# Kernel tuning notes

Hardware: AMD Instinct MI355X
Metric: run time of the kernel (lower is better)

## Reference

```python
import jax, jax.numpy as jnp
import numpy as np

DIM = 512
HEADS = 8
DIM_HEAD = 64
INNER = HEADS * DIM_HEAD  # 512
EPS = 1e-5
SCALE = DIM_HEAD ** (-0.5)


def setup_inputs() -> dict:
    key = jax.random.key(0)
    ks = jax.random.split(key, 12)
    B, S = 8, 1024
    x = jax.random.normal(ks[0], (B, DIM, S, 1), dtype=jnp.float32)
    # BatchNorm2d params (eval mode: running stats)
    bn_gamma = jax.random.normal(ks[1], (DIM,), dtype=jnp.float32) * 0.1 + 1.0
    bn_beta = jax.random.normal(ks[2], (DIM,), dtype=jnp.float32) * 0.1
    bn_mean = jax.random.normal(ks[3], (DIM,), dtype=jnp.float32) * 0.1
    bn_var = jax.random.uniform(ks[4], (DIM,), dtype=jnp.float32, minval=0.5, maxval=1.5)
    # 1x1 Conv2d == linear: weight [out, in], bias [out]
    def lin(k, out_d, in_d):
        kw, kb = jax.random.split(k)
        lim = 1.0 / np.sqrt(in_d)
        w = jax.random.uniform(kw, (out_d, in_d), dtype=jnp.float32, minval=-lim, maxval=lim)
        b = jax.random.uniform(kb, (out_d,), dtype=jnp.float32, minval=-lim, maxval=lim)
        return w, b
    wq, bq = lin(ks[5], INNER, DIM)
    wk, bk = lin(ks[6], INNER, DIM)
    wv, bv = lin(ks[7], INNER, DIM)
    wo, bo = lin(ks[8], DIM, INNER)
    return {"x": x, "bn_gamma": bn_gamma, "bn_beta": bn_beta,
            "bn_mean": bn_mean, "bn_var": bn_var,
            "wq": wq, "bq": bq, "wk": wk, "bk": bk,
            "wv": wv, "bv": bv, "wo": wo, "bo": bo}


def reference(x, bn_gamma, bn_beta, bn_mean, bn_var,
              wq, bq, wk, bk, wv, bv, wo, bo):
    B, C, S, _ = x.shape
    # BatchNorm2d (eval) over channel dim
    inv = jax.lax.rsqrt(bn_var + EPS)
    xn = (x - bn_mean[None, :, None, None]) * (bn_gamma * inv)[None, :, None, None] \
         + bn_beta[None, :, None, None]
    t = jnp.transpose(xn[..., 0], (0, 2, 1))  # [B, S, C]
    q = (t @ wq.T + bq).reshape(B, S, HEADS, DIM_HEAD)
    k = (t @ wk.T + bk).reshape(B, S, HEADS, DIM_HEAD)
    v = (t @ wv.T + bv).reshape(B, S, HEADS, DIM_HEAD)
    scores = jnp.einsum('bshd,bthd->bhst', q, k) * SCALE  # [B,H,S,S]
    attn = jax.nn.softmax(scores, axis=-1)
    o = jnp.einsum('bhst,bthd->bshd', attn, v).reshape(B, S, INNER)
    y = o @ wo.T + bo  # [B, S, C]
    return jnp.transpose(y, (0, 2, 1))[..., None]  # [B, C, S, 1]
```

## Files before the change

### kernel.cpp

```cpp
#include <hip/hip_runtime.h>
#include <stdint.h>

typedef __bf16 bf16;
typedef bf16 bf16x8 __attribute__((ext_vector_type(8)));
typedef bf16 bf16x4 __attribute__((ext_vector_type(4)));
typedef float f32x4 __attribute__((ext_vector_type(4)));
typedef float f32x16 __attribute__((ext_vector_type(16)));

#define NB 8
#define NS 1024
#define NC 512
#define NH 8
#define ND 64

#define QSCALE 0.18033688011f

__device__ __forceinline__ void gload16(const void* g, void* l) {
  __builtin_amdgcn_global_load_lds(
      (const __attribute__((address_space(1))) void*)g,
      (__attribute__((address_space(3))) void*)l, 16, 0, 0);
}

__device__ __forceinline__ unsigned pk2(float lo, float hi) {
  union { bf16 h[2]; unsigned u; } c;
  c.h[0] = (bf16)lo;
  c.h[1] = (bf16)hi;
  return c.u;
}

__device__ __forceinline__ void plswap(unsigned& x, unsigned& y) {
#if __has_builtin(__builtin_amdgcn_permlane32_swap)
  typedef unsigned uint2v __attribute__((ext_vector_type(2)));
  uint2v r = __builtin_amdgcn_permlane32_swap(x, y, false, false);
  x = r[0];
  y = r[1];
#else
  const bool hi = (threadIdx.x & 32) != 0;
  const unsigned xs = (unsigned)__shfl_xor((int)x, 32);
  const unsigned ys = (unsigned)__shfl_xor((int)y, 32);
  const unsigned nx = hi ? ys : x;
  const unsigned ny = hi ? y : xs;
  x = nx;
  y = ny;
#endif
}

__global__ __launch_bounds__(256) void prep_kernel(
    const float* __restrict__ x, const float* __restrict__ gam,
    const float* __restrict__ bet, const float* __restrict__ mu,
    const float* __restrict__ var, const float* __restrict__ wq,
    const float* __restrict__ wk, const float* __restrict__ wv,
    const float* __restrict__ wo, bf16* __restrict__ t, bf16* __restrict__ wqb,
    bf16* __restrict__ wkb, bf16* __restrict__ wvb, bf16* __restrict__ wob) {
  __shared__ float tile[32][33];
  const int bid = blockIdx.x;
  if (bid < 4096) {
    const int b = bid >> 9, c0 = ((bid >> 5) & 15) << 5, s0 = (bid & 31) << 5;
    const int tx = threadIdx.x, sj = tx & 31, ci = tx >> 5;
#pragma unroll
    for (int kk = 0; kk < 4; ++kk) {
      const int c = c0 + ci + (kk << 3);
      const float sc = gam[c] * rsqrtf(var[c] + 1e-5f);
      const float sh = bet[c] - mu[c] * sc;
      tile[ci + (kk << 3)][sj] = x[(size_t)(b * NC + c) * NS + s0 + sj] * sc + sh;
    }
    __syncthreads();
#pragma unroll
    for (int kk = 0; kk < 4; ++kk) {
      const int s = s0 + ci + (kk << 3);
      t[(size_t)(b * NS + s) * NC + c0 + sj] = (bf16)tile[sj][ci + (kk << 3)];
    }
  } else {
    const int i = ((bid - 4096) * 256 + threadIdx.x) * 4;
    float4 a = *(const float4*)(&wq[i]);
    float4 b = *(const float4*)(&wk[i]);
    float4 c = *(const float4*)(&wv[i]);
    float4 d = *(const float4*)(&wo[i]);
    bf16x4 av = {(bf16)a.x, (bf16)a.y, (bf16)a.z, (bf16)a.w};
    bf16x4 bv = {(bf16)b.x, (bf16)b.y, (bf16)b.z, (bf16)b.w};
    bf16x4 cv = {(bf16)c.x, (bf16)c.y, (bf16)c.z, (bf16)c.w};
    bf16x4 dv = {(bf16)d.x, (bf16)d.y, (bf16)d.z, (bf16)d.w};
    *(bf16x4*)(&wqb[i]) = av;
    *(bf16x4*)(&wkb[i]) = bv;
    *(bf16x4*)(&wvb[i]) = cv;
    *(bf16x4*)(&wob[i]) = dv;
  }
}

__global__ __launch_bounds__(256) void gemm_qkv_kernel(
    const bf16* __restrict__ t, const bf16* __restrict__ wqb,
    const bf16* __restrict__ wkb, const bf16* __restrict__ wvb,
    const float* __restrict__ bq, const float* __restrict__ bk,
    const float* __restrict__ bv, bf16* __restrict__ qo, bf16* __restrict__ ko,
    bf16* __restrict__ vo) {
  __shared__ __align__(16) bf16 As[2][128 * 32];
  __shared__ __align__(16) bf16 Bs[2][128 * 32];
  const int lid = blockIdx.x;
  const int xcd = lid & 7, rr = lid >> 3;
  const int ny = rr % 12, mx = (rr / 12) * 8 + xcd;
  const int m0 = mx << 7, n0 = ny << 7;
  const int tid = threadIdx.x;
  const int wsel = n0 >> 9;
  const bf16* W = (wsel == 0) ? wqb : (wsel == 1 ? wkb : wvb);
  const float* bias = (wsel == 0) ? bq : (wsel == 1 ? bk : bv);
  const int nb = n0 & 511;
  const int w = tid >> 6, lane = tid & 63, l15 = lane & 15, l4 = lane >> 4;
  const int wm = (w >> 1) << 6, wn = (w & 1) << 6;

  const int srl = lane >> 2, sp = lane & 3;
  const int r0 = w * 16 + srl, r1 = 64 + w * 16 + srl;
  const int c0off = (sp ^ ((r0 >> 1) & 3)) << 3;
  const int c1off = (sp ^ ((r1 >> 1) & 3)) << 3;
  const bf16* a0 = t + (size_t)(m0 + r0) * 512 + c0off;
  const bf16* a1 = t + (size_t)(m0 + r1) * 512 + c1off;
  const bf16* b0 = W + (size_t)(nb + r0) * 512 + c0off;
  const bf16* b1 = W + (size_t)(nb + r1) * 512 + c1off;

  f32x4 acc[4][4] = {};
  gload16(a0, &As[0][w * 512]);
  gload16(a1, &As[0][2048 + w * 512]);
  gload16(b0, &Bs[0][w * 512]);
  gload16(b1, &Bs[0][2048 + w * 512]);
  __syncthreads();
  int buf = 0;
  for (int k0 = 0; k0 < 512; k0 += 32, buf ^= 1) {
    if (k0 + 32 < 512) {
      gload16(a0 + k0 + 32, &As[buf ^ 1][w * 512]);
      gload16(a1 + k0 + 32, &As[buf ^ 1][2048 + w * 512]);
      gload16(b0 + k0 + 32, &Bs[buf ^ 1][w * 512]);
      gload16(b1 + k0 + 32, &Bs[buf ^ 1][2048 + w * 512]);
    }
    bf16x8 af[4], bfv[4];
#pragma unroll
    for (int mi = 0; mi < 4; ++mi) {
      const int row = wm + mi * 16 + l15;
      af[mi] = *(const bf16x8*)(&As[buf][row * 32 + ((l4 ^ ((row >> 1) & 3)) << 3)]);
    }
#pragma unroll
    for (int ni = 0; ni < 4; ++ni) {
      const int row = wn + ni * 16 + l15;
      bfv[ni] = *(const bf16x8*)(&Bs[buf][row * 32 + ((l4 ^ ((row >> 1) & 3)) << 3)]);
    }
    if (wsel == 2) {
#pragma unroll
      for (int mi = 0; mi < 4; ++mi)
#pragma unroll
        for (int ni = 0; ni < 4; ++ni)
          acc[mi][ni] = __builtin_amdgcn_mfma_f32_16x16x32_bf16(
              af[mi], bfv[ni], acc[mi][ni], 0, 0, 0);
    } else {
#pragma unroll
      for (int mi = 0; mi < 4; ++mi)
#pragma unroll
        for (int ni = 0; ni < 4; ++ni)
          acc[mi][ni] = __builtin_amdgcn_mfma_f32_16x16x32_bf16(
              bfv[ni], af[mi], acc[mi][ni], 0, 0, 0);
    }
    __syncthreads();
  }
  const int bidx = m0 >> 10;
  if (wsel == 2) {
    const int sbase = (m0 & 1023) + wm + (l4 << 2);
#pragma unroll
    for (int ni = 0; ni < 4; ++ni) {
      const int nn = nb + wn + ni * 16 + l15;
      const int hh = nn >> 6, dd = nn & 63;
      const float bsv = bias[nn];
      bf16* vbase = vo + (size_t)(bidx * NH + hh) * (ND * NS) + (size_t)dd * NS + sbase;
#pragma unroll
      for (int mi = 0; mi < 4; ++mi) {
        bf16x4 pk;
#pragma unroll
        for (int r = 0; r < 4; ++r) pk[r] = (bf16)(acc[mi][ni][r] + bsv);
        *(bf16x4*)(&vbase[mi * 16]) = pk;
      }
    }
  } else {
    const bool isq = (wsel == 0);
    bf16* outp = isq ? qo : ko;
    const int sbase = (m0 & 1023) + wm + l15;
#pragma unroll
    for (int ni = 0; ni < 4; ++ni) {
      const int nn0 = nb + wn + ni * 16 + (l4 << 2);
      const int hh = nn0 >> 6, dd0 = nn0 & 63;
      const float4 bs4 = *(const float4*)(&bias[nn0]);
      bf16* obase = outp + (size_t)(bidx * NH + hh) * (NS * ND) + dd0;
#pragma unroll
      for (int mi = 0; mi < 4; ++mi) {
        bf16x4 pk;
        const float* bp = (const float*)&bs4;
#pragma unroll
        for (int r = 0; r < 4; ++r) {
          float val = acc[mi][ni][r] + bp[r];
          if (isq) val *= QSCALE;
          pk[r] = (bf16)val;
        }
        *(bf16x4*)(&obase[(size_t)(sbase + mi * 16) * ND]) = pk;
      }
    }
  }
}

__global__ __launch_bounds__(256, 2) void attn_kernel(
    const bf16* __restrict__ qg, const bf16* __restrict__ kg,
    const bf16* __restrict__ vtg, bf16* __restrict__ og) {
  __shared__ __align__(16) bf16 Kb[2][64 * 64];
  __shared__ __align__(16) bf16 Vb[2][64 * 64];
  const int lid = blockIdx.x;
  const int xcd = lid & 7, rr = lid >> 3;
  const int bh = ((rr & 7) << 3) + xcd;
  const int q0 = (rr >> 3) << 7;
  const int tid = threadIdx.x, w = tid >> 6, lane = tid & 63;
  const int l31 = lane & 31, hi = lane >> 5;
  const bf16* Qp = qg + ((size_t)bh * NS + q0) * ND;
  const bf16* Kp = kg + (size_t)bh * NS * ND;
  const bf16* Vp = vtg + (size_t)bh * ND * NS;

  bf16x8 qf0, qf1, qf2, qf3;
  {
    const bf16* qrow = Qp + (size_t)(w * 32 + l31) * ND + hi * 8;
    qf0 = *(const bf16x8*)(qrow);
    qf1 = *(const bf16x8*)(qrow + 16);
    qf2 = *(const bf16x8*)(qrow + 32);
    qf3 = *(const bf16x8*)(qrow + 48);
  }

  const int srow = w * 16 + (lane >> 3);
  const int sslot = (lane & 7) ^ (srow & 7);
  const bf16* ksrc = Kp + (size_t)srow * ND + sslot * 8;
  const bf16* vsrc = Vp + (size_t)srow * NS + sslot * 8;

  f32x16 oacc0 = {}, oacc1 = {};
  float mrun = -1e30f, lrun = 0.f;

  gload16(ksrc, &Kb[0][w * 1024]);
  gload16(ksrc + 8 * ND, &Kb[0][w * 1024 + 512]);
  gload16(vsrc, &Vb[0][w * 1024]);
  gload16(vsrc + 8 * NS, &Vb[0][w * 1024 + 512]);
  __syncthreads();

  const int s7 = l31 & 7;
  int buf = 0;
  for (int kv0 = 0; kv0 < NS; kv0 += 64, buf ^= 1) {
    if (kv0 + 64 < NS) {
      gload16(ksrc + (size_t)(kv0 + 64) * ND, &Kb[buf ^ 1][w * 1024]);
      gload16(ksrc + (size_t)(kv0 + 72) * ND, &Kb[buf ^ 1][w * 1024 + 512]);
      gload16(vsrc + kv0 + 64, &Vb[buf ^ 1][w * 1024]);
      gload16(vsrc + 8 * NS + kv0 + 64, &Vb[buf ^ 1][w * 1024 + 512]);
    }
    const bf16* Ks = Kb[buf];
    const bf16* Vs = Vb[buf];
    f32x16 st0 = {}, st1 = {};
    __builtin_amdgcn_s_setprio(1);
#pragma unroll
    for (int ks = 0; ks < 4; ++ks) {
      const int sl = ((2 * ks + hi) ^ s7) << 3;
      const bf16x8 a0 = *(const bf16x8*)(&Ks[l31 * 64 + sl]);
      const bf16x8 a1 = *(const bf16x8*)(&Ks[(32 + l31) * 64 + sl]);
      const bf16x8 qk = (ks == 0) ? qf0 : (ks == 1) ? qf1 : (ks == 2) ? qf2 : qf3;
      st0 = __builtin_amdgcn_mfma_f32_32x32x16_bf16(a0, qk, st0, 0, 0, 0);
      st1 = __builtin_amdgcn_mfma_f32_32x32x16_bf16(a1, qk, st1, 0, 0, 0);
    }
    __builtin_amdgcn_s_setprio(0);
    float pm = st0[0];
#pragma unroll
    for (int i = 1; i < 16; ++i) pm = fmaxf(pm, st0[i]);
#pragma unroll
    for (int i = 0; i < 16; ++i) pm = fmaxf(pm, st1[i]);
    pm = fmaxf(pm, __shfl_xor(pm, 32));
    if (!__all(pm - mrun <= 8.f)) {
      const float mnew = fmaxf(mrun, pm);
      const float alpha = __builtin_amdgcn_exp2f(mrun - mnew);
#pragma unroll
      for (int i = 0; i < 16; ++i) {
        oacc0[i] *= alpha;
        oacc1[i] *= alpha;
      }
      lrun *= alpha;
      mrun = mnew;
    }
    float rs = 0.f;
#pragma unroll
    for (int t = 0; t < 4; ++t) {
      float p[8];
#pragma unroll
      for (int i = 0; i < 8; ++i) {
        const float sv = (t < 2) ? st0[8 * (t & 1) + i] : st1[8 * (t & 1) + i];
        p[i] = __builtin_amdgcn_exp2f(sv - mrun);
        rs += p[i];
      }
      unsigned c01 = pk2(p[0], p[1]), c23 = pk2(p[2], p[3]);
      unsigned c45 = pk2(p[4], p[5]), c67 = pk2(p[6], p[7]);
      plswap(c01, c45);
      plswap(c23, c67);
      union { unsigned u[4]; bf16x8 v; } pu;
      pu.u[0] = c01;
      pu.u[1] = c23;
      pu.u[2] = c45;
      pu.u[3] = c67;
      const int sl = ((2 * t + hi) ^ s7) << 3;
      const bf16x8 v0 = *(const bf16x8*)(&Vs[l31 * 64 + sl]);
      const bf16x8 v1 = *(const bf16x8*)(&Vs[(32 + l31) * 64 + sl]);
      __builtin_amdgcn_s_setprio(1);
      oacc0 = __builtin_amdgcn_mfma_f32_32x32x16_bf16(v0, pu.v, oacc0, 0, 0, 0);
      oacc1 = __builtin_amdgcn_mfma_f32_32x32x16_bf16(v1, pu.v, oacc1, 0, 0, 0);
      __builtin_amdgcn_s_setprio(0);
    }
    lrun += rs;
    __syncthreads();
  }
  lrun += __shfl_xor(lrun, 32);
  const float linv = 1.f / lrun;
  const int b = bh >> 3, h = bh & 7;
  bf16* Op = og + (size_t)(b * NS + q0 + w * 32 + l31) * NC + h * ND;
#pragma unroll
  for (int g = 0; g < 4; ++g) {
    bf16x4 pk0, pk1;
#pragma unroll
    for (int r = 0; r < 4; ++r) {
      pk0[r] = (bf16)(oacc0[4 * g + r] * linv);
      pk1[r] = (bf16)(oacc1[4 * g + r] * linv);
    }
    *(bf16x4*)(&Op[g * 8 + 4 * hi]) = pk0;
    *(bf16x4*)(&Op[32 + g * 8 + 4 * hi]) = pk1;
  }
}

__global__ __launch_bounds__(256) void gemm_out_kernel(
    const bf16* __restrict__ wob, const bf16* __restrict__ o,
    const float* __restrict__ bo, float* __restrict__ out) {
  __shared__ __align__(16) bf16 As[2][64 * 32];
  __shared__ __align__(16) bf16 Bs[2][128 * 32];
  const int lid = blockIdx.x;
  const int xcd = lid & 7, rr = lid >> 3;
  const int mx = rr & 7, ny = ((rr >> 3) << 3) + xcd;
  const int m0 = mx << 6, n0 = ny << 7;
  const int tid = threadIdx.x;
  const int w = tid >> 6, lane = tid & 63, l15 = lane & 15, l4 = lane >> 4;
  const int wm = (w >> 1) << 5;
  const int wn = (w & 1) << 6;

  const int srl = lane >> 2, sp = lane & 3;
  const int ra = w * 16 + srl;
  const int caoff = (sp ^ ((ra >> 1) & 3)) << 3;
  const bf16* a0 = wob + (size_t)(m0 + ra) * 512 + caoff;
  const int rb0 = w * 16 + srl, rb1 = 64 + w * 16 + srl;
  const int cb0off = (sp ^ ((rb0 >> 1) & 3)) << 3;
  const int cb1off = (sp ^ ((rb1 >> 1) & 3)) << 3;
  const bf16* b0 = o + (size_t)(n0 + rb0) * 512 + cb0off;
  const bf16* b1 = o + (size_t)(n0 + rb1) * 512 + cb1off;

  f32x4 acc[2][4] = {};
  gload16(a0, &As[0][w * 512]);
  gload16(b0, &Bs[0][w * 512]);
  gload16(b1, &Bs[0][2048 + w * 512]);
  __syncthreads();
  int buf = 0;
  for (int k0 = 0; k0 < 512; k0 += 32, buf ^= 1) {
    if (k0 + 32 < 512) {
      gload16(a0 + k0 + 32, &As[buf ^ 1][w * 512]);
      gload16(b0 + k0 + 32, &Bs[buf ^ 1][w * 512]);
      gload16(b1 + k0 + 32, &Bs[buf ^ 1][2048 + w * 512]);
    }
    bf16x8 af[2], bfv[4];
#pragma unroll
    for (int mi = 0; mi < 2; ++mi) {
      const int row = wm + mi * 16 + l15;
      af[mi] = *(const bf16x8*)(&As[buf][row * 32 + ((l4 ^ ((row >> 1) & 3)) << 3)]);
    }
#pragma unroll
    for (int ni = 0; ni < 4; ++ni) {
      const int row = wn + ni * 16 + l15;
      bfv[ni] = *(const bf16x8*)(&Bs[buf][row * 32 + ((l4 ^ ((row >> 1) & 3)) << 3)]);
    }
#pragma unroll
    for (int mi = 0; mi < 2; ++mi)
#pragma unroll
      for (int ni = 0; ni < 4; ++ni)
        acc[mi][ni] = __builtin_amdgcn_mfma_f32_16x16x32_bf16(
            bfv[ni], af[mi], acc[mi][ni], 0, 0, 0);
    __syncthreads();
  }
  const int b = n0 >> 10;
  const int sb = (n0 & 1023) + wn;
#pragma unroll
  for (int mi = 0; mi < 2; ++mi) {
    const int cout = m0 + wm + mi * 16 + l15;
    const float bsv = bo[cout];
    float* obase = out + (size_t)(b * NC + cout) * NS;
#pragma unroll
    for (int ni = 0; ni < 4; ++ni) {
      const int s0i = sb + ni * 16 + (l4 << 2);
      float4 pk = {acc[mi][ni][0] + bsv, acc[mi][ni][1] + bsv,
                   acc[mi][ni][2] + bsv, acc[mi][ni][3] + bsv};
      *(float4*)(&obase[s0i]) = pk;
    }
  }
}

extern "C" void kernel_launch(void* const* d_in, const int* in_sizes, int n_in,
                              void* d_out, int out_size, void* d_ws,
                              size_t ws_size, hipStream_t stream) {
  const float* x = (const float*)d_in[0];
  const float* gam = (const float*)d_in[1];
  const float* bet = (const float*)d_in[2];
  const float* mu = (const float*)d_in[3];
  const float* var = (const float*)d_in[4];
  const float* wq = (const float*)d_in[5];
  const float* bq = (const float*)d_in[6];
  const float* wk = (const float*)d_in[7];
  const float* bk = (const float*)d_in[8];
  const float* wv = (const float*)d_in[9];
  const float* bv = (const float*)d_in[10];
  const float* wo = (const float*)d_in[11];
  const float* bo = (const float*)d_in[12];
  float* out = (float*)d_out;

  char* p = (char*)d_ws;
  const size_t big = (size_t)8192 * 512 * sizeof(bf16);
  bf16* t = (bf16*)p;   p += big;
  bf16* q = (bf16*)p;   p += big;
  bf16* k = (bf16*)p;   p += big;
  bf16* vt = (bf16*)p;  p += big;
  const size_t wsz = (size_t)512 * 512 * sizeof(bf16);
  bf16* wqb = (bf16*)p; p += wsz;
  bf16* wkb = (bf16*)p; p += wsz;
  bf16* wvb = (bf16*)p; p += wsz;
  bf16* wob = (bf16*)p; p += wsz;
  bf16* o = t;

  prep_kernel<<<dim3(4352), 256, 0, stream>>>(x, gam, bet, mu, var, wq, wk, wv,
                                              wo, t, wqb, wkb, wvb, wob);
  gemm_qkv_kernel<<<dim3(768), 256, 0, stream>>>(t, wqb, wkb, wvb, bq, bk, bv,
                                                 q, k, vt);
  attn_kernel<<<dim3(512), 256, 0, stream>>>(q, k, vt, o);
  gemm_out_kernel<<<dim3(512), 256, 0, stream>>>(wob, o, bo, out);
}
```

Baseline: 86.43 us.

## Load K/V fragments directly from global into registers in attention, drop LDS staging

The attention kernel no longer stages K and V tiles in shared memory with double buffering and barriers. Each wave now loads its MFMA operand fragments straight from global memory into registers, prefetching the next K tile during softmax with ping-pong register arrays. The aim is to remove LDS traffic and __syncthreads, but each of the four waves now fetches the same K/V data separately, which raises global/L2 traffic and register pressure. The QKV GEMM also gets a launch-bounds occupancy hint of 3.

```diff
diff --git a/kernel.cpp b/kernel.cpp
--- a/kernel.cpp
+++ b/kernel.cpp
@@ -87,7 +87,7 @@
   }
 }
 
-__global__ __launch_bounds__(256) void gemm_qkv_kernel(
+__global__ __launch_bounds__(256, 3) void gemm_qkv_kernel(
     const bf16* __restrict__ t, const bf16* __restrict__ wqb,
     const bf16* __restrict__ wkb, const bf16* __restrict__ wvb,
     const float* __restrict__ bq, const float* __restrict__ bk,
@@ -204,8 +204,6 @@
 __global__ __launch_bounds__(256, 2) void attn_kernel(
     const bf16* __restrict__ qg, const bf16* __restrict__ kg,
     const bf16* __restrict__ vtg, bf16* __restrict__ og) {
-  __shared__ __align__(16) bf16 Kb[2][64 * 64];
-  __shared__ __align__(16) bf16 Vb[2][64 * 64];
   const int lid = blockIdx.x;
   const int xcd = lid & 7, rr = lid >> 3;
   const int bh = ((rr & 7) << 3) + xcd;
@@ -213,55 +211,50 @@
   const int tid = threadIdx.x, w = tid >> 6, lane = tid & 63;
   const int l31 = lane & 31, hi = lane >> 5;
   const bf16* Qp = qg + ((size_t)bh * NS + q0) * ND;
-  const bf16* Kp = kg + (size_t)bh * NS * ND;
-  const bf16* Vp = vtg + (size_t)bh * ND * NS;
-
-  bf16x8 qf0, qf1, qf2, qf3;
+  const bf16* kb = kg + (size_t)bh * NS * ND + (size_t)l31 * ND + hi * 8;
+  const bf16* vb = vtg + (size_t)bh * ND * NS + (size_t)l31 * NS + hi * 8;
+  const bf16* vb2 = vb + (size_t)32 * NS;
+
+  bf16x8 qf[4];
   {
     const bf16* qrow = Qp + (size_t)(w * 32 + l31) * ND + hi * 8;
-    qf0 = *(const bf16x8*)(qrow);
-    qf1 = *(const bf16x8*)(qrow + 16);
-    qf2 = *(const bf16x8*)(qrow + 32);
-    qf3 = *(const bf16x8*)(qrow + 48);
-  }
-
-  const int srow = w * 16 + (lane >> 3);
-  const int sslot = (lane & 7) ^ (srow & 7);
-  const bf16* ksrc = Kp + (size_t)srow * ND + sslot * 8;
-  const bf16* vsrc = Vp + (size_t)srow * NS + sslot * 8;
+#pragma unroll
+    for (int ks = 0; ks < 4; ++ks) qf[ks] = *(const bf16x8*)(qrow + ks * 16);
+  }
 
   f32x16 oacc0 = {}, oacc1 = {};
   float mrun = -1e30f, lrun = 0.f;
 
-  gload16(ksrc, &Kb[0][w * 1024]);
-  gload16(ksrc + 8 * ND, &Kb[0][w * 1024 + 512]);
-  gload16(vsrc, &Vb[0][w * 1024]);
-  gload16(vsrc + 8 * NS, &Vb[0][w * 1024 + 512]);
-  __syncthreads();
-
-  const int s7 = l31 & 7;
-  int buf = 0;
-  for (int kv0 = 0; kv0 < NS; kv0 += 64, buf ^= 1) {
-    if (kv0 + 64 < NS) {
-      gload16(ksrc + (size_t)(kv0 + 64) * ND, &Kb[buf ^ 1][w * 1024]);
-      gload16(ksrc + (size_t)(kv0 + 72) * ND, &Kb[buf ^ 1][w * 1024 + 512]);
-      gload16(vsrc + kv0 + 64, &Vb[buf ^ 1][w * 1024]);
-      gload16(vsrc + 8 * NS + kv0 + 64, &Vb[buf ^ 1][w * 1024 + 512]);
-    }
-    const bf16* Ks = Kb[buf];
-    const bf16* Vs = Vb[buf];
+  bf16x8 kA0[4], kA1[4], kB0[4], kB1[4];
+#pragma unroll
+  for (int ks = 0; ks < 4; ++ks) {
+    kA0[ks] = *(const bf16x8*)(kb + ks * 16);
+    kA1[ks] = *(const bf16x8*)(kb + (size_t)32 * ND + ks * 16);
+  }
+
+  auto tile = [&](const bf16x8 (&kc0)[4], const bf16x8 (&kc1)[4],
+                  bf16x8 (&kn0)[4], bf16x8 (&kn1)[4], int kv0) {
+    bf16x8 vf0[4], vf1[4];
+#pragma unroll
+    for (int t = 0; t < 4; ++t) {
+      vf0[t] = *(const bf16x8*)(vb + kv0 + t * 16);
+      vf1[t] = *(const bf16x8*)(vb2 + kv0 + t * 16);
+    }
     f32x16 st0 = {}, st1 = {};
     __builtin_amdgcn_s_setprio(1);
 #pragma unroll
     for (int ks = 0; ks < 4; ++ks) {
-      const int sl = ((2 * ks + hi) ^ s7) << 3;
-      const bf16x8 a0 = *(const bf16x8*)(&Ks[l31 * 64 + sl]);
-      const bf16x8 a1 = *(const bf16x8*)(&Ks[(32 + l31) * 64 + sl]);
-      const bf16x8 qk = (ks == 0) ? qf0 : (ks == 1) ? qf1 : (ks == 2) ? qf2 : qf3;
-      st0 = __builtin_amdgcn_mfma_f32_32x32x16_bf16(a0, qk, st0, 0, 0, 0);
-      st1 = __builtin_amdgcn_mfma_f32_32x32x16_bf16(a1, qk, st1, 0, 0, 0);
+      st0 = __builtin_amdgcn_mfma_f32_32x32x16_bf16(kc0[ks], qf[ks], st0, 0, 0, 0);
+      st1 = __builtin_amdgcn_mfma_f32_32x32x16_bf16(kc1[ks], qf[ks], st1, 0, 0, 0);
     }
     __builtin_amdgcn_s_setprio(0);
+    if (kv0 + 64 < NS) {
+#pragma unroll
+      for (int ks = 0; ks < 4; ++ks) {
+        kn0[ks] = *(const bf16x8*)(kb + (size_t)(kv0 + 64) * ND + ks * 16);
+        kn1[ks] = *(const bf16x8*)(kb + (size_t)(kv0 + 96) * ND + ks * 16);
+      }
+    }
     float pm = st0[0];
 #pragma unroll
     for (int i = 1; i < 16; ++i) pm = fmaxf(pm, st0[i]);
@@ -298,17 +291,19 @@
       pu.u[1] = c23;
       pu.u[2] = c45;
       pu.u[3] = c67;
-      const int sl = ((2 * t + hi) ^ s7) << 3;
-      const bf16x8 v0 = *(const bf16x8*)(&Vs[l31 * 64 + sl]);
-      const bf16x8 v1 = *(const bf16x8*)(&Vs[(32 + l31) * 64 + sl]);
       __builtin_amdgcn_s_setprio(1);
-      oacc0 = __builtin_amdgcn_mfma_f32_32x32x16_bf16(v0, pu.v, oacc0, 0, 0, 0);
-      oacc1 = __builtin_amdgcn_mfma_f32_32x32x16_bf16(v1, pu.v, oacc1, 0, 0, 0);
+      oacc0 = __builtin_amdgcn_mfma_f32_32x32x16_bf16(vf0[t], pu.v, oacc0, 0, 0, 0);
+      oacc1 = __builtin_amdgcn_mfma_f32_32x32x16_bf16(vf1[t], pu.v, oacc1, 0, 0, 0);
       __builtin_amdgcn_s_setprio(0);
     }
     lrun += rs;
-    __syncthreads();
-  }
+  };
+
+  for (int kv0 = 0; kv0 < NS; kv0 += 128) {
+    tile(kA0, kA1, kB0, kB1, kv0);
+    tile(kB0, kB1, kA0, kA1, kv0 + 64);
+  }
+
   lrun += __shfl_xor(lrun, 32);
   const float linv = 1.f / lrun;
   const int b = bh >> 3, h = bh & 7;
```

Measured after the change: 114.0 us. +31.9%, slower.

## Split KV range across two wave groups in attention and merge partials via LDS

Applied to the files above, without the earlier changes.

The attention kernel launches 512 threads per block: two groups of four waves each process half of the key/value sequence with their own double-buffered LDS tiles. The second group writes its running max, sum and output accumulators to LDS, and the first group rescales and merges them before writing the output. This halves the serial KV loop per query tile and raises wave count per block, at the cost of doubled LDS per block, an extra combine phase and sync. The QKV GEMM also gets a min-blocks-per-CU launch bound hint.

```diff
diff --git a/kernel.cpp b/kernel.cpp
--- a/kernel.cpp
+++ b/kernel.cpp
@@ -87,7 +87,7 @@
   }
 }
 
-__global__ __launch_bounds__(256) void gemm_qkv_kernel(
+__global__ __launch_bounds__(256, 3) void gemm_qkv_kernel(
     const bf16* __restrict__ t, const bf16* __restrict__ wqb,
     const bf16* __restrict__ wkb, const bf16* __restrict__ wvb,
     const float* __restrict__ bq, const float* __restrict__ bk,
@@ -201,31 +201,29 @@
   }
 }
 
-__global__ __launch_bounds__(256, 2) void attn_kernel(
+__global__ __launch_bounds__(512, 4) void attn_kernel(
     const bf16* __restrict__ qg, const bf16* __restrict__ kg,
     const bf16* __restrict__ vtg, bf16* __restrict__ og) {
-  __shared__ __align__(16) bf16 Kb[2][64 * 64];
-  __shared__ __align__(16) bf16 Vb[2][64 * 64];
+  __shared__ __align__(16) bf16 KVs[2][2][2][64 * 64];
   const int lid = blockIdx.x;
   const int xcd = lid & 7, rr = lid >> 3;
   const int bh = ((rr & 7) << 3) + xcd;
   const int q0 = (rr >> 3) << 7;
   const int tid = threadIdx.x, w = tid >> 6, lane = tid & 63;
+  const int wq = w & 3, wkv = w >> 2;
   const int l31 = lane & 31, hi = lane >> 5;
   const bf16* Qp = qg + ((size_t)bh * NS + q0) * ND;
-  const bf16* Kp = kg + (size_t)bh * NS * ND;
-  const bf16* Vp = vtg + (size_t)bh * ND * NS;
-
-  bf16x8 qf0, qf1, qf2, qf3;
+  const bf16* Kp = kg + ((size_t)bh * NS + wkv * 512) * ND;
+  const bf16* Vp = vtg + (size_t)bh * ND * NS + wkv * 512;
+
+  bf16x8 qf[4];
   {
-    const bf16* qrow = Qp + (size_t)(w * 32 + l31) * ND + hi * 8;
-    qf0 = *(const bf16x8*)(qrow);
-    qf1 = *(const bf16x8*)(qrow + 16);
-    qf2 = *(const bf16x8*)(qrow + 32);
-    qf3 = *(const bf16x8*)(qrow + 48);
-  }
-
-  const int srow = w * 16 + (lane >> 3);
+    const bf16* qrow = Qp + (size_t)(wq * 32 + l31) * ND + hi * 8;
+#pragma unroll
+    for (int ks = 0; ks < 4; ++ks) qf[ks] = *(const bf16x8*)(qrow + ks * 16);
+  }
+
+  const int srow = wq * 16 + (lane >> 3);
   const int sslot = (lane & 7) ^ (srow & 7);
   const bf16* ksrc = Kp + (size_t)srow * ND + sslot * 8;
   const bf16* vsrc = Vp + (size_t)srow * NS + sslot * 8;
@@ -233,23 +231,24 @@
   f32x16 oacc0 = {}, oacc1 = {};
   float mrun = -1e30f, lrun = 0.f;
 
-  gload16(ksrc, &Kb[0][w * 1024]);
-  gload16(ksrc + 8 * ND, &Kb[0][w * 1024 + 512]);
-  gload16(vsrc, &Vb[0][w * 1024]);
-  gload16(vsrc + 8 * NS, &Vb[0][w * 1024 + 512]);
+  gload16(ksrc, &KVs[wkv][0][0][wq * 1024]);
+  gload16(ksrc + 8 * ND, &KVs[wkv][0][0][wq * 1024 + 512]);
+  gload16(vsrc, &KVs[wkv][1][0][wq * 1024]);
+  gload16(vsrc + 8 * NS, &KVs[wkv][1][0][wq * 1024 + 512]);
   __syncthreads();
 
   const int s7 = l31 & 7;
   int buf = 0;
-  for (int kv0 = 0; kv0 < NS; kv0 += 64, buf ^= 1) {
-    if (kv0 + 64 < NS) {
-      gload16(ksrc + (size_t)(kv0 + 64) * ND, &Kb[buf ^ 1][w * 1024]);
-      gload16(ksrc + (size_t)(kv0 + 72) * ND, &Kb[buf ^ 1][w * 1024 + 512]);
-      gload16(vsrc + kv0 + 64, &Vb[buf ^ 1][w * 1024]);
-      gload16(vsrc + 8 * NS + kv0 + 64, &Vb[buf ^ 1][w * 1024 + 512]);
-    }
-    const bf16* Ks = Kb[buf];
-    const bf16* Vs = Vb[buf];
+  for (int kv0 = 0; kv0 < 512; kv0 += 64, buf ^= 1) {
+    if (kv0 + 64 < 512) {
+      gload16(ksrc + (size_t)(kv0 + 64) * ND, &KVs[wkv][0][buf ^ 1][wq * 1024]);
+      gload16(ksrc + (size_t)(kv0 + 72) * ND,
+              &KVs[wkv][0][buf ^ 1][wq * 1024 + 512]);
+      gload16(vsrc + kv0 + 64, &KVs[wkv][1][buf ^ 1][wq * 1024]);
+      gload16(vsrc + 8 * NS + kv0 + 64, &KVs[wkv][1][buf ^ 1][wq * 1024 + 512]);
+    }
+    const bf16* Ks = KVs[wkv][0][buf];
+    const bf16* Vs = KVs[wkv][1][buf];
     f32x16 st0 = {}, st1 = {};
     __builtin_amdgcn_s_setprio(1);
 #pragma unroll
@@ -257,9 +256,8 @@
       const int sl = ((2 * ks + hi) ^ s7) << 3;
       const bf16x8 a0 = *(const bf16x8*)(&Ks[l31 * 64 + sl]);
       const bf16x8 a1 = *(const bf16x8*)(&Ks[(32 + l31) * 64 + sl]);
-      const bf16x8 qk = (ks == 0) ? qf0 : (ks == 1) ? qf1 : (ks == 2) ? qf2 : qf3;
-      st0 = __builtin_amdgcn_mfma_f32_32x32x16_bf16(a0, qk, st0, 0, 0, 0);
-      st1 = __builtin_amdgcn_mfma_f32_32x32x16_bf16(a1, qk, st1, 0, 0, 0);
+      st0 = __builtin_amdgcn_mfma_f32_32x32x16_bf16(a0, qf[ks], st0, 0, 0, 0);
+      st1 = __builtin_amdgcn_mfma_f32_32x32x16_bf16(a1, qf[ks], st1, 0, 0, 0);
     }
     __builtin_amdgcn_s_setprio(0);
     float pm = st0[0];
@@ -310,19 +308,42 @@
     __syncthreads();
   }
   lrun += __shfl_xor(lrun, 32);
-  const float linv = 1.f / lrun;
-  const int b = bh >> 3, h = bh & 7;
-  bf16* Op = og + (size_t)(b * NS + q0 + w * 32 + l31) * NC + h * ND;
-#pragma unroll
-  for (int g = 0; g < 4; ++g) {
-    bf16x4 pk0, pk1;
-#pragma unroll
-    for (int r = 0; r < 4; ++r) {
-      pk0[r] = (bf16)(oacc0[4 * g + r] * linv);
-      pk1[r] = (bf16)(oacc1[4 * g + r] * linv);
-    }
-    *(bf16x4*)(&Op[g * 8 + 4 * hi]) = pk0;
-    *(bf16x4*)(&Op[32 + g * 8 + 4 * hi]) = pk1;
+
+  float* comb = (float*)&KVs[0][0][0][0];
+  if (wkv == 1) {
+    const int base = wq * 34 * 64;
+    comb[base + lane] = mrun;
+    comb[base + 64 + lane] = lrun;
+#pragma unroll
+    for (int i = 0; i < 16; ++i) {
+      comb[base + (2 + i) * 64 + lane] = oacc0[i];
+      comb[base + (18 + i) * 64 + lane] = oacc1[i];
+    }
+  }
+  __syncthreads();
+  if (wkv == 0) {
+    const int base = wq * 34 * 64;
+    const float mb = comb[base + lane];
+    const float lb = comb[base + 64 + lane];
+    const float m = fmaxf(mrun, mb);
+    const float aa = __builtin_amdgcn_exp2f(mrun - m);
+    const float ab = __builtin_amdgcn_exp2f(mb - m);
+    const float linv = 1.f / (lrun * aa + lb * ab);
+    const int b = bh >> 3, h = bh & 7;
+    bf16* Op = og + (size_t)(b * NS + q0 + wq * 32 + l31) * NC + h * ND;
+#pragma unroll
+    for (int g = 0; g < 4; ++g) {
+      bf16x4 pk0, pk1;
+#pragma unroll
+      for (int r = 0; r < 4; ++r) {
+        const float ob0 = comb[base + (2 + 4 * g + r) * 64 + lane];
+        const float ob1 = comb[base + (18 + 4 * g + r) * 64 + lane];
+        pk0[r] = (bf16)((oacc0[4 * g + r] * aa + ob0 * ab) * linv);
+        pk1[r] = (bf16)((oacc1[4 * g + r] * aa + ob1 * ab) * linv);
+      }
+      *(bf16x4*)(&Op[g * 8 + 4 * hi]) = pk0;
+      *(bf16x4*)(&Op[32 + g * 8 + 4 * hi]) = pk1;
+    }
   }
 }
 
@@ -433,6 +454,6 @@
                                               wo, t, wqb, wkb, wvb, wob);
   gemm_qkv_kernel<<<dim3(768), 256, 0, stream>>>(t, wqb, wkb, wvb, bq, bk, bv,
                                                  q, k, vt);
-  attn_kernel<<<dim3(512), 256, 0, stream>>>(q, k, vt, o);
+  attn_kernel<<<dim3(512), 512, 0, stream>>>(q, k, vt, o);
   gemm_out_kernel<<<dim3(512), 256, 0, stream>>>(wob, o, bo, out);
 }
```

Measured after the change: 79.92 us. 1.08x faster.
